# Kernel optimization log

Measured on AMD Instinct MI355X. Metric: run time of the kernel, lower is better.

## Reference

```python
import jax, jax.numpy as jnp
import numpy as np

B, H, N, D = 2, 8, 2048, 64


def setup_inputs() -> dict:
    key = jax.random.key(0)
    kq, kk, kv = jax.random.split(key, 3)
    q = jax.random.normal(kq, (B, H, N, D), dtype=jnp.float32)
    k = jax.random.normal(kk, (B, H, N, D), dtype=jnp.float32)
    v = jax.random.normal(kv, (B, H, N, D), dtype=jnp.float32)
    return {"q": q, "k": k, "v": v}


def _selective_attn(sim):
    # sim: (b, h, i, j). Gate computed from first head, relu'd, SOS unmasked,
    # diagonal zeroed, shifted down one row, cumsum over query rows, subtracted.
    b, h, i, j = sim.shape
    gate = jax.nn.relu(sim[:, 0])                       # (b, i, j)
    gate = gate.at[:, :, j - i].set(0.0)                # no_mask_sos: column -i
    eye = jnp.eye(i, dtype=sim.dtype)
    if j > i:
        eye = jnp.pad(eye, ((0, 0), (j - i, 0)), constant_values=1.0)
    gate = (1.0 - eye) * gate
    # F.pad(gate, (0,0,1,-1)): shift rows down by one, drop last row
    gate = jnp.pad(gate, ((0, 0), (1, 0), (0, 0)))[:, :i, :]
    gate = jnp.cumsum(gate, axis=-2)
    return sim - gate[:, None]                          # broadcast over heads


def reference(q, k, v):
    scale = q.shape[-1] ** -0.5
    i, j = q.shape[-2], k.shape[-2]

    # squared L2 distance scores: ||q||^2 + ||k||^2 - 2 q.k  (== cdist(q,k)**2)
    q_sq = jnp.sum(q * q, axis=-1)                      # (b, h, i)
    k_sq = jnp.sum(k * k, axis=-1)                      # (b, h, j)
    qk = jnp.einsum('bhid,bhjd->bhij', q, k)            # (b, h, i, j)
    d2 = jnp.maximum(q_sq[..., :, None] + k_sq[..., None, :] - 2.0 * qk, 0.0)
    sim = -d2 * scale

    # causal mask (triu with offset j - i + 1)
    mask_value = -jnp.finfo(sim.dtype).max
    causal = jnp.triu(jnp.ones((i, j), dtype=bool), j - i + 1)
    sim = jnp.where(causal, mask_value, sim)

    # selective attention gating
    sim = _selective_attn(sim)

    # one-hot straight-through attention
    idx = jnp.argmax(sim, axis=-1)                      # (b, h, i)
    hard = jax.nn.one_hot(idx, j, dtype=sim.dtype)      # (b, h, i, j)
    soft = jax.nn.softmax(sim, axis=-1)
    attn = hard + soft - jax.lax.stop_gradient(soft)

    return jnp.einsum('bhij,bhjd->bhid', attn, v)
```

## Files before the change

### kernel.cpp

```cpp
#include <hip/hip_runtime.h>
#include <stdint.h>

#define B_ 2
#define H_ 8
#define N_ 2048
#define D_ 64
#define BH_ (B_ * H_)
#define NROWS (BH_ * N_)
#define TPB_ 544
#define TASKS (TPB_ * BH_)
#define EPSF 8e-3f
#define INFF __int_as_float(0x7f800000)

using u64 = unsigned long long;
using u32 = unsigned int;
typedef __attribute__((ext_vector_type(8))) short short8;
typedef __attribute__((ext_vector_type(4))) float f32x4;

#define MFMA16(A, B, C) __builtin_amdgcn_mfma_f32_16x16x32_bf16((A), (B), (C), 0, 0, 0)

__global__ __launch_bounds__(256) void prep_k(
    const float* __restrict__ k, char* __restrict__ khi_g,
    char* __restrict__ klo_g, float* __restrict__ ksq_g,
    u32* __restrict__ count)
{
  if (blockIdx.x == 0 && threadIdx.x == 0) count[0] = 0;
  const int t = (int)blockIdx.x * 256 + threadIdx.x;
  const int r = t >> 3, kg = t & 7;
  const float* kp = k + (size_t)r * D_ + kg * 8;
  const float4 f0 = *(const float4*)kp;
  const float4 f1 = *(const float4*)(kp + 4);
  const float vv[8] = {f0.x, f0.y, f0.z, f0.w, f1.x, f1.y, f1.z, f1.w};
  u32 hw[4], lw[4];
  float ps = 0.f;
  #pragma unroll
  for (int e = 0; e < 4; ++e) {
    const float va = vv[2 * e], vb = vv[2 * e + 1];
    ps = fmaf(va, va, ps); ps = fmaf(vb, vb, ps);
    const u32 ha = __float_as_uint(va) & 0xFFFF0000u;
    const u32 hb = __float_as_uint(vb) & 0xFFFF0000u;
    hw[e] = (ha >> 16) | hb;
    const u32 la = __float_as_uint(va - __uint_as_float(ha));
    const u32 lb = __float_as_uint(vb - __uint_as_float(hb));
    lw[e] = (la >> 16) | (lb & 0xFFFF0000u);
  }
  const size_t off = ((size_t)(r >> 4) * 2 + (kg >> 2)) * 1024 +
                     (size_t)(((kg & 3) << 4) + (r & 15)) * 16;
  *(uint4*)(khi_g + off) = make_uint4(hw[0], hw[1], hw[2], hw[3]);
  *(uint4*)(klo_g + off) = make_uint4(lw[0], lw[1], lw[2], lw[3]);
  float ssum = ps;
  ssum += __shfl_xor(ssum, 1);
  ssum += __shfl_xor(ssum, 2);
  ssum += __shfl_xor(ssum, 4);
  if (kg == 0) ksq_g[r] = ssum;
}

__device__ __forceinline__ void cvt_hilo(const float* p, short8& hi, short8& lo) {
  const float4 f0 = *(const float4*)p;
  const float4 f1 = *(const float4*)(p + 4);
  const float vv[8] = {f0.x, f0.y, f0.z, f0.w, f1.x, f1.y, f1.z, f1.w};
  #pragma unroll
  for (int e = 0; e < 8; ++e) {
    const float v = vv[e];
    const u32 hb = __float_as_uint(v) & 0xFFFF0000u;
    hi[e] = (short)(hb >> 16);
    lo[e] = (short)(__float_as_uint(v - __uint_as_float(hb)) >> 16);
  }
}

__global__ __launch_bounds__(64, 4) void phase1(
    const float* __restrict__ q, const char* __restrict__ khi_g,
    const char* __restrict__ klo_g, const float* __restrict__ ksq_g,
    u64* __restrict__ bestc, u32* __restrict__ secc)
{
  const int b = (int)blockIdx.x;
  const int task = (b & 7) * (TASKS / 8) + (b >> 3);
  const int bh = task / TPB_;
  const int rem = task - bh * TPB_;
  int a = 0;
  while (2 * (a + 1) * (a + 2) <= rem) ++a;
  const int idx = rem - 2 * a * (a + 1);
  const int g2 = 4 * a + idx / (a + 1);
  const int c = idx - (idx / (a + 1)) * (a + 1);
  const int jfirst = c * 8;
  const int jlast = min(jfirst + 7, 2 * g2 + 1);

  const int lane = threadIdx.x & 63;
  const int grp = lane >> 4, c0 = lane & 15;
  const int i0 = g2 * 32;

  short8 ah00, ah01, al00, al01, ah10, ah11, al10, al11;
  {
    const float* q0 = q + ((size_t)bh * N_ + i0 + c0) * D_ + grp * 8;
    cvt_hilo(q0, ah00, al00);
    cvt_hilo(q0 + 32, ah01, al01);
    const float* q1 = q0 + 16 * D_;
    cvt_hilo(q1, ah10, al10);
    cvt_hilo(q1 + 32, ah11, al11);
  }

  float bf[2][4], sf[2][4];
  u32 bj[2][4];
  #pragma unroll
  for (int s = 0; s < 2; ++s)
    #pragma unroll
    for (int r2 = 0; r2 < 4; ++r2) {
      bf[s][r2] = INFF; sf[s][r2] = INFF; bj[s][r2] = 0;
    }

  const size_t fb = (size_t)bh * 128 * 2048;
  const char* ph = khi_g + fb + (size_t)jfirst * 2048 + lane * 16;
  const char* pl = klo_g + fb + (size_t)jfirst * 2048 + lane * 16;
  const float* pk = ksq_g + (size_t)bh * N_ + jfirst * 16 + c0;

  short8 ch0 = *(const short8*)(ph);
  short8 ch1 = *(const short8*)(ph + 1024);
  short8 cl0 = *(const short8*)(pl);
  short8 cl1 = *(const short8*)(pl + 1024);
  float cks = *pk;

  for (int js = jfirst; js <= jlast; ++js) {
    const int adv = (js < jlast) ? 1 : 0;
    const short8 nh0 = *(const short8*)(ph + adv * 2048);
    const short8 nh1 = *(const short8*)(ph + adv * 2048 + 1024);
    const short8 nl0 = *(const short8*)(pl + adv * 2048);
    const short8 nl1 = *(const short8*)(pl + adv * 2048 + 1024);
    const float nks = pk[adv * 16];
    ph += adv * 2048; pl += adv * 2048; pk += adv * 16;

    const int jcol = js * 16 + c0;
    if (js <= 2 * g2) {
      const bool dsub = (js == 2 * g2);
      f32x4 aA = {0.f, 0.f, 0.f, 0.f}, aB = {0.f, 0.f, 0.f, 0.f};
      aA = MFMA16(ah00, ch0, aA);  aB = MFMA16(ah01, ch1, aB);
      aA = MFMA16(ah00, cl0, aA);  aB = MFMA16(ah01, cl1, aB);
      aA = MFMA16(al00, ch0, aA);  aB = MFMA16(al01, ch1, aB);
      #pragma unroll
      for (int reg = 0; reg < 4; ++reg) {
        float score = fmaf(-2.f, aA[reg] + aB[reg], cks);
        if (dsub && jcol > i0 + grp * 4 + reg) score = INFF;
        const float loser = fmaxf(bf[0][reg], score);
        sf[0][reg] = fminf(sf[0][reg], loser);
        if (score < bf[0][reg]) bj[0][reg] = (u32)jcol;
        bf[0][reg] = fminf(bf[0][reg], score);
      }
    }
    {
      const bool dsub = (js == 2 * g2 + 1);
      f32x4 aA = {0.f, 0.f, 0.f, 0.f}, aB = {0.f, 0.f, 0.f, 0.f};
      aA = MFMA16(ah10, ch0, aA);  aB = MFMA16(ah11, ch1, aB);
      aA = MFMA16(ah10, cl0, aA);  aB = MFMA16(ah11, cl1, aB);
      aA = MFMA16(al10, ch0, aA);  aB = MFMA16(al11, ch1, aB);
      #pragma unroll
      for (int reg = 0; reg < 4; ++reg) {
        float score = fmaf(-2.f, aA[reg] + aB[reg], cks);
        if (dsub && jcol > i0 + 16 + grp * 4 + reg) score = INFF;
        const float loser = fmaxf(bf[1][reg], score);
        sf[1][reg] = fminf(sf[1][reg], loser);
        if (score < bf[1][reg]) bj[1][reg] = (u32)jcol;
        bf[1][reg] = fminf(bf[1][reg], score);
      }
    }
    ch0 = nh0; ch1 = nh1; cl0 = nl0; cl1 = nl1; cks = nks;
  }

  #pragma unroll
  for (int s = 0; s < 2; ++s) {
    #pragma unroll
    for (int reg = 0; reg < 4; ++reg) {
      const u32 bbits = __float_as_uint(bf[s][reg]);
      const u32 key = bbits ^ (u32)(((int)bbits >> 31) | 0x80000000);
      u64 pkk = ((u64)key << 32) | bj[s][reg];
      float sv = sf[s][reg];
      #pragma unroll
      for (int m = 1; m < 16; m <<= 1) {
        const u64 opk = (u64)__shfl_xor((long long)pkk, m);
        const float osv = __shfl_xor(sv, m);
        const u32 mk = (u32)(pkk >> 32), ok = (u32)(opk >> 32);
        const u32 lk = (opk < pkk) ? mk : ok;
        const u32 lb = (lk & 0x80000000u) ? (lk ^ 0x80000000u) : ~lk;
        sv = fminf(fminf(sv, osv), __uint_as_float(lb));
        if (opk < pkk) pkk = opk;
      }
      if (c0 == 0) {
        const size_t rr = (size_t)bh * N_ + i0 + s * 16 + grp * 4 + reg;
        bestc[(size_t)c * NROWS + rr] = pkk;
        secc[(size_t)c * NROWS + rr] = __float_as_uint(sv);
      }
    }
  }
}

__global__ __launch_bounds__(256) void combine_gather(
    const u64* __restrict__ bestc, const u32* __restrict__ secc,
    const float* __restrict__ v, float* __restrict__ out,
    u32* __restrict__ flaglist, u32* __restrict__ count)
{
  __shared__ u64 pk_s[4][64];
  __shared__ float s1_s[4][64];
  __shared__ u32 idx_s[64];
  const int tid = threadIdx.x;
  const int r0 = (int)blockIdx.x * 64;
  const int p = tid >> 6, t6 = tid & 63;

  {
    const int r = r0 + t6;
    const int i = r & (N_ - 1);
    const int nch = (2 * (i >> 5) + 9) >> 3;
    u64 b0 = ~0ull;
    float bcur = INFF, s1 = INFF;
    int cstar = -1;
    for (int c2 = p; c2 < nch; c2 += 4) {
      const u64 kk = bestc[(size_t)c2 * NROWS + r];
      const u32 key = (u32)(kk >> 32);
      const u32 bits = (key & 0x80000000u) ? (key ^ 0x80000000u) : ~key;
      const float f = __uint_as_float(bits);
      if (kk < b0) { s1 = fminf(s1, bcur); b0 = kk; bcur = f; cstar = c2; }
      else s1 = fminf(s1, f);
    }
    if (cstar >= 0)
      s1 = fminf(s1, __uint_as_float(secc[(size_t)cstar * NROWS + r]));
    pk_s[p][t6] = b0;
    s1_s[p][t6] = s1;
  }
  __syncthreads();

  if (tid < 64) {
    u64 b0 = ~0ull;
    float bcur = INFF, s1 = INFF;
    #pragma unroll
    for (int pp = 0; pp < 4; ++pp) {
      const u64 kk = pk_s[pp][tid];
      const u32 key = (u32)(kk >> 32);
      const u32 bits = (key & 0x80000000u) ? (key ^ 0x80000000u) : ~key;
      const float f = __uint_as_float(bits);
      if (kk < b0) { s1 = fminf(s1, bcur); b0 = kk; bcur = f; }
      else s1 = fminf(s1, f);
      s1 = fminf(s1, s1_s[pp][tid]);
    }
    idx_s[tid] = (u32)(b0 & 0xFFFFu);
    if ((s1 - bcur) < EPSF) {
      const u32 pos = atomicAdd(count, 1u);
      flaglist[pos] = (u32)(r0 + tid);
    }
  }
  __syncthreads();

  #pragma unroll
  for (int iter = 0; iter < 4; ++iter) {
    const int tk = tid + iter * 256;
    const int rl = tk >> 4, cc = tk & 15;
    const int r = r0 + rl;
    const u32 j = idx_s[rl];
    const int bh = r >> 11;
    const float4 val = ((const float4*)(v + ((size_t)bh * N_ + j) * D_))[cc];
    ((float4*)(out + (size_t)r * D_))[cc] = val;
  }
}

__global__ __launch_bounds__(64) void exact_partial(
    const float* __restrict__ q, const float* __restrict__ k,
    const u32* __restrict__ flaglist, const u32* __restrict__ count,
    double* __restrict__ pd, int* __restrict__ pj)
{
  const int lane = threadIdx.x & 63;
  const int cnt = (int)count[0];
  for (int t = blockIdx.x; (t >> 4) < cnt; t += (int)gridDim.x) {
    const int li = t >> 4, slice = t & 15;
    const int r = (int)flaglist[li];
    const int bh = r >> 11;
    const int i = r & (N_ - 1);
    const int jbase = slice * 128;

    double bbest = 1e300;
    int bjj = 0x7FFFFFFF;
    if (jbase <= i) {
      const float4* qr = (const float4*)(q + (size_t)r * D_);
      float4 qv[16];
      #pragma unroll
      for (int t2 = 0; t2 < 16; ++t2) qv[t2] = qr[t2];
      double s0 = 0, s1 = 0, s2 = 0, s3 = 0;
      #pragma unroll
      for (int t2 = 0; t2 < 16; ++t2) {
        s0 = fma((double)qv[t2].x, (double)qv[t2].x, s0);
        s1 = fma((double)qv[t2].y, (double)qv[t2].y, s1);
        s2 = fma((double)qv[t2].z, (double)qv[t2].z, s2);
        s3 = fma((double)qv[t2].w, (double)qv[t2].w, s3);
      }
      const double qsqd = (s0 + s1) + (s2 + s3);
      const float* kb = k + (size_t)bh * N_ * D_;

      #pragma unroll
      for (int u = 0; u < 2; ++u) {
        const int j = jbase + u * 64 + lane;
        if (j <= i) {
          const float4* kr = (const float4*)(kb + (size_t)j * D_);
          double a0 = 0, a1 = 0, a2 = 0, a3 = 0;
          double t0 = 0, t1 = 0, t2d = 0, t3 = 0;
          #pragma unroll
          for (int t2 = 0; t2 < 16; ++t2) {
            const float4 kv = kr[t2];
            const double k0 = kv.x, k1 = kv.y, k2 = kv.z, k3 = kv.w;
            a0 = fma((double)qv[t2].x, k0, a0);
            a1 = fma((double)qv[t2].y, k1, a1);
            a2 = fma((double)qv[t2].z, k2, a2);
            a3 = fma((double)qv[t2].w, k3, a3);
            t0 = fma(k0, k0, t0);
            t1 = fma(k1, k1, t1);
            t2d = fma(k2, k2, t2d);
            t3 = fma(k3, k3, t3);
          }
          const double raw = (qsqd + ((t0 + t1) + (t2d + t3))) -
                             2.0 * ((a0 + a1) + (a2 + a3));
          const double d2 = raw > 0.0 ? raw : 0.0;
          if (d2 < bbest) { bbest = d2; bjj = j; }
        }
      }
      #pragma unroll
      for (int m = 1; m < 64; m <<= 1) {
        const double ob = __shfl_xor(bbest, m);
        const int oj = __shfl_xor(bjj, m);
        if (ob < bbest || (ob == bbest && oj < bjj)) { bbest = ob; bjj = oj; }
      }
    }
    if (lane == 0) {
      pd[(size_t)li * 16 + slice] = bbest;
      pj[(size_t)li * 16 + slice] = bjj;
    }
  }
}

__global__ __launch_bounds__(64) void exact_final(
    const double* __restrict__ pd, const int* __restrict__ pj,
    const u32* __restrict__ flaglist, const u32* __restrict__ count,
    const float* __restrict__ v, float* __restrict__ out)
{
  const int lane = threadIdx.x & 63;
  const int cnt = (int)count[0];
  for (int li = blockIdx.x; li < cnt; li += (int)gridDim.x) {
    const int r = (int)flaglist[li];
    const int bh = r >> 11;
    double d = (lane < 16) ? pd[(size_t)li * 16 + lane] : 1e300;
    int j = (lane < 16) ? pj[(size_t)li * 16 + lane] : 0x7FFFFFFF;
    #pragma unroll
    for (int m = 1; m < 16; m <<= 1) {
      const double od = __shfl_xor(d, m);
      const int oj = __shfl_xor(j, m);
      if (od < d || (od == d && oj < j)) { d = od; j = oj; }
    }
    if (lane < 16) {
      const float4 val =
          ((const float4*)(v + ((size_t)bh * N_ + j) * D_))[lane];
      ((float4*)(out + (size_t)r * D_))[lane] = val;
    }
  }
}

extern "C" void kernel_launch(void* const* d_in, const int* in_sizes, int n_in,
                              void* d_out, int out_size, void* d_ws,
                              size_t ws_size, hipStream_t stream) {
  const float* q = (const float*)d_in[0];
  const float* k = (const float*)d_in[1];
  const float* v = (const float*)d_in[2];
  float* out = (float*)d_out;

  char* ws = (char*)d_ws;
  u32* count = (u32*)ws;
  u32* flaglist = (u32*)(ws + 4096);
  float* ksq_g = (float*)(ws + 256 * 1024);
  char* khi_g = ws + 1ull * 1024 * 1024;
  char* klo_g = ws + 8ull * 1024 * 1024;
  u64* bestc = (u64*)(ws + 16ull * 1024 * 1024);
  u32* secc = (u32*)(ws + 24ull * 1024 * 1024);
  double* pd = (double*)(ws + 32ull * 1024 * 1024);
  int* pj = (int*)(ws + 40ull * 1024 * 1024);

  prep_k<<<(NROWS * 8) / 256, 256, 0, stream>>>(k, khi_g, klo_g, ksq_g, count);
  phase1<<<TASKS, 64, 0, stream>>>(q, khi_g, klo_g, ksq_g, bestc, secc);
  combine_gather<<<NROWS / 64, 256, 0, stream>>>(bestc, secc, v, out,
                                                 flaglist, count);
  exact_partial<<<2048, 64, 0, stream>>>(q, k, flaglist, count, pd, pj);
  exact_final<<<256, 64, 0, stream>>>(pd, pj, flaglist, count, v, out);
}
```

Measured before the change: 56.79 us.

## Widen phase1 query tile from 32 to 64 rows per wave

Each phase1 wavefront now handles 64 query rows (four 16-row MFMA subtiles) instead of 32, so every K chunk loaded from global memory is reused across twice as many rows. This halves the task count per head and changes the triangular task decomposition and the chunk count used by combine_gather. The cost is more registers for the Q fragments and running best/second state, so the occupancy hint drops from 4 to 3 waves, and there are fewer blocks to keep the GPU busy.

```diff
diff --git a/kernel.cpp b/kernel.cpp
--- a/kernel.cpp
+++ b/kernel.cpp
@@ -7,7 +7,7 @@
 #define D_ 64
 #define BH_ (B_ * H_)
 #define NROWS (BH_ * N_)
-#define TPB_ 544
+#define TPB_ 272
 #define TASKS (TPB_ * BH_)
 #define EPSF 8e-3f
 #define INFF __int_as_float(0x7f800000)
@@ -68,7 +68,7 @@
   }
 }
 
-__global__ __launch_bounds__(64, 4) void phase1(
+__global__ __launch_bounds__(64, 3) void phase1(
     const float* __restrict__ q, const char* __restrict__ khi_g,
     const char* __restrict__ klo_g, const float* __restrict__ ksq_g,
     u64* __restrict__ bestc, u32* __restrict__ secc)
@@ -77,32 +77,32 @@
   const int task = (b & 7) * (TASKS / 8) + (b >> 3);
   const int bh = task / TPB_;
   const int rem = task - bh * TPB_;
-  int a = 0;
-  while (2 * (a + 1) * (a + 2) <= rem) ++a;
-  const int idx = rem - 2 * a * (a + 1);
-  const int g2 = 4 * a + idx / (a + 1);
-  const int c = idx - (idx / (a + 1)) * (a + 1);
+  int t = 0;
+  while ((t + 1) * (t + 2) <= rem) ++t;
+  const int idx = rem - t * (t + 1);
+  const int qn = idx / (t + 1);
+  const int g4 = 2 * t + qn;
+  const int c = idx - qn * (t + 1);
   const int jfirst = c * 8;
-  const int jlast = min(jfirst + 7, 2 * g2 + 1);
+  const int jlast = min(jfirst + 7, 4 * g4 + 3);
 
   const int lane = threadIdx.x & 63;
   const int grp = lane >> 4, c0 = lane & 15;
-  const int i0 = g2 * 32;
-
-  short8 ah00, ah01, al00, al01, ah10, ah11, al10, al11;
-  {
-    const float* q0 = q + ((size_t)bh * N_ + i0 + c0) * D_ + grp * 8;
-    cvt_hilo(q0, ah00, al00);
-    cvt_hilo(q0 + 32, ah01, al01);
-    const float* q1 = q0 + 16 * D_;
-    cvt_hilo(q1, ah10, al10);
-    cvt_hilo(q1 + 32, ah11, al11);
-  }
-
-  float bf[2][4], sf[2][4];
-  u32 bj[2][4];
-  #pragma unroll
-  for (int s = 0; s < 2; ++s)
+  const int i0 = g4 * 64;
+
+  short8 ah[4][2], al[4][2];
+  #pragma unroll
+  for (int s = 0; s < 4; ++s) {
+    const float* qrow =
+        q + ((size_t)bh * N_ + i0 + s * 16 + c0) * D_ + grp * 8;
+    cvt_hilo(qrow, ah[s][0], al[s][0]);
+    cvt_hilo(qrow + 32, ah[s][1], al[s][1]);
+  }
+
+  float bf[4][4], sf[4][4];
+  u32 bj[4][4];
+  #pragma unroll
+  for (int s = 0; s < 4; ++s)
     #pragma unroll
     for (int r2 = 0; r2 < 4; ++r2) {
       bf[s][r2] = INFF; sf[s][r2] = INFF; bj[s][r2] = 0;
@@ -129,43 +129,29 @@
     ph += adv * 2048; pl += adv * 2048; pk += adv * 16;
 
     const int jcol = js * 16 + c0;
-    if (js <= 2 * g2) {
-      const bool dsub = (js == 2 * g2);
+    #pragma unroll
+    for (int s = 0; s < 4; ++s) {
+      if (js > 4 * g4 + s) continue;
+      const bool dsub = (js == 4 * g4 + s);
       f32x4 aA = {0.f, 0.f, 0.f, 0.f}, aB = {0.f, 0.f, 0.f, 0.f};
-      aA = MFMA16(ah00, ch0, aA);  aB = MFMA16(ah01, ch1, aB);
-      aA = MFMA16(ah00, cl0, aA);  aB = MFMA16(ah01, cl1, aB);
-      aA = MFMA16(al00, ch0, aA);  aB = MFMA16(al01, ch1, aB);
+      aA = MFMA16(ah[s][0], ch0, aA);  aB = MFMA16(ah[s][1], ch1, aB);
+      aA = MFMA16(ah[s][0], cl0, aA);  aB = MFMA16(ah[s][1], cl1, aB);
+      aA = MFMA16(al[s][0], ch0, aA);  aB = MFMA16(al[s][1], ch1, aB);
       #pragma unroll
       for (int reg = 0; reg < 4; ++reg) {
         float score = fmaf(-2.f, aA[reg] + aB[reg], cks);
-        if (dsub && jcol > i0 + grp * 4 + reg) score = INFF;
-        const float loser = fmaxf(bf[0][reg], score);
-        sf[0][reg] = fminf(sf[0][reg], loser);
-        if (score < bf[0][reg]) bj[0][reg] = (u32)jcol;
-        bf[0][reg] = fminf(bf[0][reg], score);
-      }
-    }
-    {
-      const bool dsub = (js == 2 * g2 + 1);
-      f32x4 aA = {0.f, 0.f, 0.f, 0.f}, aB = {0.f, 0.f, 0.f, 0.f};
-      aA = MFMA16(ah10, ch0, aA);  aB = MFMA16(ah11, ch1, aB);
-      aA = MFMA16(ah10, cl0, aA);  aB = MFMA16(ah11, cl1, aB);
-      aA = MFMA16(al10, ch0, aA);  aB = MFMA16(al11, ch1, aB);
-      #pragma unroll
-      for (int reg = 0; reg < 4; ++reg) {
-        float score = fmaf(-2.f, aA[reg] + aB[reg], cks);
-        if (dsub && jcol > i0 + 16 + grp * 4 + reg) score = INFF;
-        const float loser = fmaxf(bf[1][reg], score);
-        sf[1][reg] = fminf(sf[1][reg], loser);
-        if (score < bf[1][reg]) bj[1][reg] = (u32)jcol;
-        bf[1][reg] = fminf(bf[1][reg], score);
+        if (dsub && jcol > i0 + s * 16 + grp * 4 + reg) score = INFF;
+        const float loser = fmaxf(bf[s][reg], score);
+        sf[s][reg] = fminf(sf[s][reg], loser);
+        if (score < bf[s][reg]) bj[s][reg] = (u32)jcol;
+        bf[s][reg] = fminf(bf[s][reg], score);
       }
     }
     ch0 = nh0; ch1 = nh1; cl0 = nl0; cl1 = nl1; cks = nks;
   }
 
   #pragma unroll
-  for (int s = 0; s < 2; ++s) {
+  for (int s = 0; s < 4; ++s) {
     #pragma unroll
     for (int reg = 0; reg < 4; ++reg) {
       const u32 bbits = __float_as_uint(bf[s][reg]);
@@ -206,7 +192,7 @@
   {
     const int r = r0 + t6;
     const int i = r & (N_ - 1);
-    const int nch = (2 * (i >> 5) + 9) >> 3;
+    const int nch = ((i >> 6) + 2) >> 1;
     u64 b0 = ~0ull;
     float bcur = INFF, s1 = INFF;
     int cstar = -1;
```

After: 62.82 us. +10.6%, slower.

## Precompute Q bf16 hi/lo fragments and double key chunk size per task

Applied to the files above, without the earlier changes.

The prep kernel now also converts Q into MFMA-ready bf16 hi/lo fragments in workspace, so phase1 loads them directly instead of converting per task. Each phase1 task now covers 16 key tiles instead of 8, which roughly halves the task count (TPB 544 to 288) and the number of partial results combine_gather has to merge. The launch-bounds occupancy hint drops from 4 to 3 waves to leave room for more registers. Longer tasks may worsen load balance across the triangular causal work and add an extra Q write/read pass.

```diff
diff --git a/kernel.cpp b/kernel.cpp
--- a/kernel.cpp
+++ b/kernel.cpp
@@ -7,7 +7,7 @@
 #define D_ 64
 #define BH_ (B_ * H_)
 #define NROWS (BH_ * N_)
-#define TPB_ 544
+#define TPB_ 288
 #define TASKS (TPB_ * BH_)
 #define EPSF 8e-3f
 #define INFF __int_as_float(0x7f800000)
@@ -19,85 +19,103 @@
 
 #define MFMA16(A, B, C) __builtin_amdgcn_mfma_f32_16x16x32_bf16((A), (B), (C), 0, 0, 0)
 
-__global__ __launch_bounds__(256) void prep_k(
-    const float* __restrict__ k, char* __restrict__ khi_g,
-    char* __restrict__ klo_g, float* __restrict__ ksq_g,
+__global__ __launch_bounds__(256) void prep_all(
+    const float* __restrict__ q, const float* __restrict__ k,
+    char* __restrict__ khi_g, char* __restrict__ klo_g,
+    float* __restrict__ ksq_g, char* __restrict__ qfrag,
     u32* __restrict__ count)
 {
-  if (blockIdx.x == 0 && threadIdx.x == 0) count[0] = 0;
-  const int t = (int)blockIdx.x * 256 + threadIdx.x;
-  const int r = t >> 3, kg = t & 7;
-  const float* kp = k + (size_t)r * D_ + kg * 8;
-  const float4 f0 = *(const float4*)kp;
-  const float4 f1 = *(const float4*)(kp + 4);
-  const float vv[8] = {f0.x, f0.y, f0.z, f0.w, f1.x, f1.y, f1.z, f1.w};
-  u32 hw[4], lw[4];
-  float ps = 0.f;
-  #pragma unroll
-  for (int e = 0; e < 4; ++e) {
-    const float va = vv[2 * e], vb = vv[2 * e + 1];
-    ps = fmaf(va, va, ps); ps = fmaf(vb, vb, ps);
-    const u32 ha = __float_as_uint(va) & 0xFFFF0000u;
-    const u32 hb = __float_as_uint(vb) & 0xFFFF0000u;
-    hw[e] = (ha >> 16) | hb;
-    const u32 la = __float_as_uint(va - __uint_as_float(ha));
-    const u32 lb = __float_as_uint(vb - __uint_as_float(hb));
-    lw[e] = (la >> 16) | (lb & 0xFFFF0000u);
-  }
-  const size_t off = ((size_t)(r >> 4) * 2 + (kg >> 2)) * 1024 +
-                     (size_t)(((kg & 3) << 4) + (r & 15)) * 16;
-  *(uint4*)(khi_g + off) = make_uint4(hw[0], hw[1], hw[2], hw[3]);
-  *(uint4*)(klo_g + off) = make_uint4(lw[0], lw[1], lw[2], lw[3]);
-  float ssum = ps;
-  ssum += __shfl_xor(ssum, 1);
-  ssum += __shfl_xor(ssum, 2);
-  ssum += __shfl_xor(ssum, 4);
-  if (kg == 0) ksq_g[r] = ssum;
-}
-
-__device__ __forceinline__ void cvt_hilo(const float* p, short8& hi, short8& lo) {
-  const float4 f0 = *(const float4*)p;
-  const float4 f1 = *(const float4*)(p + 4);
-  const float vv[8] = {f0.x, f0.y, f0.z, f0.w, f1.x, f1.y, f1.z, f1.w};
-  #pragma unroll
-  for (int e = 0; e < 8; ++e) {
-    const float v = vv[e];
-    const u32 hb = __float_as_uint(v) & 0xFFFF0000u;
-    hi[e] = (short)(hb >> 16);
-    lo[e] = (short)(__float_as_uint(v - __uint_as_float(hb)) >> 16);
-  }
-}
-
-__global__ __launch_bounds__(64, 4) void phase1(
-    const float* __restrict__ q, const char* __restrict__ khi_g,
+  const int blk = (int)blockIdx.x;
+  if (blk < 1024) {
+    if (blk == 0 && threadIdx.x == 0) count[0] = 0;
+    const int t = blk * 256 + threadIdx.x;
+    const int r = t >> 3, kg = t & 7;
+    const float* kp = k + (size_t)r * D_ + kg * 8;
+    const float4 f0 = *(const float4*)kp;
+    const float4 f1 = *(const float4*)(kp + 4);
+    const float vv[8] = {f0.x, f0.y, f0.z, f0.w, f1.x, f1.y, f1.z, f1.w};
+    u32 hw[4], lw[4];
+    float ps = 0.f;
+    #pragma unroll
+    for (int e = 0; e < 4; ++e) {
+      const float va = vv[2 * e], vb = vv[2 * e + 1];
+      ps = fmaf(va, va, ps); ps = fmaf(vb, vb, ps);
+      const u32 ha = __float_as_uint(va) & 0xFFFF0000u;
+      const u32 hb = __float_as_uint(vb) & 0xFFFF0000u;
+      hw[e] = (ha >> 16) | hb;
+      const u32 la = __float_as_uint(va - __uint_as_float(ha));
+      const u32 lb = __float_as_uint(vb - __uint_as_float(hb));
+      lw[e] = (la >> 16) | (lb & 0xFFFF0000u);
+    }
+    const size_t off = ((size_t)(r >> 4) * 2 + (kg >> 2)) * 1024 +
+                       (size_t)(((kg & 3) << 4) + (r & 15)) * 16;
+    *(uint4*)(khi_g + off) = make_uint4(hw[0], hw[1], hw[2], hw[3]);
+    *(uint4*)(klo_g + off) = make_uint4(lw[0], lw[1], lw[2], lw[3]);
+    float ssum = ps;
+    ssum += __shfl_xor(ssum, 1);
+    ssum += __shfl_xor(ssum, 2);
+    ssum += __shfl_xor(ssum, 4);
+    if (kg == 0) ksq_g[r] = ssum;
+  } else {
+    const int t2 = (blk - 1024) * 256 + threadIdx.x;
+    const int l = t2 & 63;
+    const int p = (t2 >> 6) & 3;
+    const int grp = (t2 >> 8) & 127;
+    const int bh = t2 >> 15;
+    const int h = p & 1, islo = p >> 1;
+    const int row = bh * N_ + grp * 16 + (l & 15);
+    const float* src = q + (size_t)row * D_ + h * 32 + (l >> 4) * 8;
+    const float4 f0 = *(const float4*)src;
+    const float4 f1 = *(const float4*)(src + 4);
+    const float vv[8] = {f0.x, f0.y, f0.z, f0.w, f1.x, f1.y, f1.z, f1.w};
+    u32 wds[4];
+    #pragma unroll
+    for (int e = 0; e < 4; ++e) {
+      const float va = vv[2 * e], vb = vv[2 * e + 1];
+      const u32 ha = __float_as_uint(va) & 0xFFFF0000u;
+      const u32 hb = __float_as_uint(vb) & 0xFFFF0000u;
+      if (islo) {
+        const u32 la = __float_as_uint(va - __uint_as_float(ha));
+        const u32 lb = __float_as_uint(vb - __uint_as_float(hb));
+        wds[e] = (la >> 16) | (lb & 0xFFFF0000u);
+      } else {
+        wds[e] = (ha >> 16) | hb;
+      }
+    }
+    const size_t off = ((((size_t)bh * 128 + grp) * 4 + p) * 64 + l) * 16;
+    *(uint4*)(qfrag + off) = make_uint4(wds[0], wds[1], wds[2], wds[3]);
+  }
+}
+
+__global__ __launch_bounds__(64, 3) void phase1(
+    const char* __restrict__ qfrag, const char* __restrict__ khi_g,
     const char* __restrict__ klo_g, const float* __restrict__ ksq_g,
     u64* __restrict__ bestc, u32* __restrict__ secc)
 {
   const int b = (int)blockIdx.x;
   const int task = (b & 7) * (TASKS / 8) + (b >> 3);
   const int bh = task / TPB_;
-  const int rem = task - bh * TPB_;
-  int a = 0;
-  while (2 * (a + 1) * (a + 2) <= rem) ++a;
-  const int idx = rem - 2 * a * (a + 1);
-  const int g2 = 4 * a + idx / (a + 1);
-  const int c = idx - (idx / (a + 1)) * (a + 1);
-  const int jfirst = c * 8;
-  const int jlast = min(jfirst + 7, 2 * g2 + 1);
+  int rem = task - bh * TPB_;
+  int g2 = 0, nc = 1;
+  while (rem >= nc) { rem -= nc; ++g2; nc = (2 * g2 + 17) >> 4; }
+  const int c = rem;
+  const int jfirst = c * 16;
+  const int jlast = min(jfirst + 15, 2 * g2 + 1);
 
   const int lane = threadIdx.x & 63;
   const int grp = lane >> 4, c0 = lane & 15;
   const int i0 = g2 * 32;
 
-  short8 ah00, ah01, al00, al01, ah10, ah11, al10, al11;
-  {
-    const float* q0 = q + ((size_t)bh * N_ + i0 + c0) * D_ + grp * 8;
-    cvt_hilo(q0, ah00, al00);
-    cvt_hilo(q0 + 32, ah01, al01);
-    const float* q1 = q0 + 16 * D_;
-    cvt_hilo(q1, ah10, al10);
-    cvt_hilo(q1 + 32, ah11, al11);
-  }
+  const char* qb =
+      qfrag + ((((size_t)bh * 128 + g2 * 2) * 4) * 64 + lane) * 16;
+  const short8 ah00 = *(const short8*)(qb);
+  const short8 ah01 = *(const short8*)(qb + 1024);
+  const short8 al00 = *(const short8*)(qb + 2048);
+  const short8 al01 = *(const short8*)(qb + 3072);
+  const short8 ah10 = *(const short8*)(qb + 4096);
+  const short8 ah11 = *(const short8*)(qb + 4096 + 1024);
+  const short8 al10 = *(const short8*)(qb + 4096 + 2048);
+  const short8 al11 = *(const short8*)(qb + 4096 + 3072);
 
   float bf[2][4], sf[2][4];
   u32 bj[2][4];
@@ -206,7 +224,7 @@
   {
     const int r = r0 + t6;
     const int i = r & (N_ - 1);
-    const int nch = (2 * (i >> 5) + 9) >> 3;
+    const int nch = (2 * (i >> 5) + 17) >> 4;
     u64 b0 = ~0ull;
     float bcur = INFF, s1 = INFF;
     int cstar = -1;
@@ -374,9 +392,10 @@
   u32* secc = (u32*)(ws + 24ull * 1024 * 1024);
   double* pd = (double*)(ws + 32ull * 1024 * 1024);
   int* pj = (int*)(ws + 40ull * 1024 * 1024);
-
-  prep_k<<<(NROWS * 8) / 256, 256, 0, stream>>>(k, khi_g, klo_g, ksq_g, count);
-  phase1<<<TASKS, 64, 0, stream>>>(q, khi_g, klo_g, ksq_g, bestc, secc);
+  char* qfrag = ws + 44ull * 1024 * 1024;
+
+  prep_all<<<3072, 256, 0, stream>>>(q, k, khi_g, klo_g, ksq_g, qfrag, count);
+  phase1<<<TASKS, 64, 0, stream>>>(qfrag, khi_g, klo_g, ksq_g, bestc, secc);
   combine_gather<<<NROWS / 64, 256, 0, stream>>>(bestc, secc, v, out,
                                                  flaglist, count);
   exact_partial<<<2048, 64, 0, stream>>>(q, k, flaglist, count, pd, pj);
```

New measurement: 56.09 us. Within noise of the previous version (-1.2%).

## Use 16-tile column chunks in phase1 and fuse exact fallback kernels

Applied to the files above, without the earlier changes.

Phase1 tasks now cover up to 16 key tiles instead of 8, which roughly halves the task count and the per-chunk candidate writes that combine_gather must merge. The task decode becomes a simple loop, and occupancy is lowered to 3 waves. The explicit register double-buffering of the next K tile is removed in favour of direct loads. The exact_partial and exact_final kernels are merged into one 1024-thread block that reduces the 16 slices through shared memory, dropping one launch and the partial-result round trip. The trade-off is less parallelism per row group in phase1 and possible load latency exposure without prefetch.

```diff
diff --git a/kernel.cpp b/kernel.cpp
--- a/kernel.cpp
+++ b/kernel.cpp
@@ -7,7 +7,7 @@
 #define D_ 64
 #define BH_ (B_ * H_)
 #define NROWS (BH_ * N_)
-#define TPB_ 544
+#define TPB_ 288
 #define TASKS (TPB_ * BH_)
 #define EPSF 8e-3f
 #define INFF __int_as_float(0x7f800000)
@@ -68,7 +68,7 @@
   }
 }
 
-__global__ __launch_bounds__(64, 4) void phase1(
+__global__ __launch_bounds__(64, 3) void phase1(
     const float* __restrict__ q, const char* __restrict__ khi_g,
     const char* __restrict__ klo_g, const float* __restrict__ ksq_g,
     u64* __restrict__ bestc, u32* __restrict__ secc)
@@ -76,14 +76,12 @@
   const int b = (int)blockIdx.x;
   const int task = (b & 7) * (TASKS / 8) + (b >> 3);
   const int bh = task / TPB_;
-  const int rem = task - bh * TPB_;
-  int a = 0;
-  while (2 * (a + 1) * (a + 2) <= rem) ++a;
-  const int idx = rem - 2 * a * (a + 1);
-  const int g2 = 4 * a + idx / (a + 1);
-  const int c = idx - (idx / (a + 1)) * (a + 1);
-  const int jfirst = c * 8;
-  const int jlast = min(jfirst + 7, 2 * g2 + 1);
+  int rem = task - bh * TPB_;
+  int g2 = 0, nc = 1;
+  while (rem >= nc) { rem -= nc; ++g2; nc = (2 * g2 + 17) >> 4; }
+  const int c = rem;
+  const int jfirst = c * 16;
+  const int jlast = min(jfirst + 15, 2 * g2 + 1);
 
   const int lane = threadIdx.x & 63;
   const int grp = lane >> 4, c0 = lane & 15;
@@ -113,20 +111,13 @@
   const char* pl = klo_g + fb + (size_t)jfirst * 2048 + lane * 16;
   const float* pk = ksq_g + (size_t)bh * N_ + jfirst * 16 + c0;
 
-  short8 ch0 = *(const short8*)(ph);
-  short8 ch1 = *(const short8*)(ph + 1024);
-  short8 cl0 = *(const short8*)(pl);
-  short8 cl1 = *(const short8*)(pl + 1024);
-  float cks = *pk;
-
   for (int js = jfirst; js <= jlast; ++js) {
-    const int adv = (js < jlast) ? 1 : 0;
-    const short8 nh0 = *(const short8*)(ph + adv * 2048);
-    const short8 nh1 = *(const short8*)(ph + adv * 2048 + 1024);
-    const short8 nl0 = *(const short8*)(pl + adv * 2048);
-    const short8 nl1 = *(const short8*)(pl + adv * 2048 + 1024);
-    const float nks = pk[adv * 16];
-    ph += adv * 2048; pl += adv * 2048; pk += adv * 16;
+    const short8 ch0 = *(const short8*)(ph);
+    const short8 ch1 = *(const short8*)(ph + 1024);
+    const short8 cl0 = *(const short8*)(pl);
+    const short8 cl1 = *(const short8*)(pl + 1024);
+    const float cks = *pk;
+    ph += 2048; pl += 2048; pk += 16;
 
     const int jcol = js * 16 + c0;
     if (js <= 2 * g2) {
@@ -161,7 +152,6 @@
         bf[1][reg] = fminf(bf[1][reg], score);
       }
     }
-    ch0 = nh0; ch1 = nh1; cl0 = nl0; cl1 = nl1; cks = nks;
   }
 
   #pragma unroll
@@ -206,7 +196,7 @@
   {
     const int r = r0 + t6;
     const int i = r & (N_ - 1);
-    const int nch = (2 * (i >> 5) + 9) >> 3;
+    const int nch = (2 * (i >> 5) + 17) >> 4;
     u64 b0 = ~0ull;
     float bcur = INFF, s1 = INFF;
     int cstar = -1;
@@ -258,19 +248,22 @@
   }
 }
 
-__global__ __launch_bounds__(64) void exact_partial(
+__global__ __launch_bounds__(1024) void exact_fused(
     const float* __restrict__ q, const float* __restrict__ k,
-    const u32* __restrict__ flaglist, const u32* __restrict__ count,
-    double* __restrict__ pd, int* __restrict__ pj)
+    const float* __restrict__ v, float* __restrict__ out,
+    const u32* __restrict__ flaglist, const u32* __restrict__ count)
 {
-  const int lane = threadIdx.x & 63;
+  __shared__ double sd[16];
+  __shared__ int sj[16];
+  const int tid = threadIdx.x;
+  const int w = tid >> 6;
+  const int lane = tid & 63;
   const int cnt = (int)count[0];
-  for (int t = blockIdx.x; (t >> 4) < cnt; t += (int)gridDim.x) {
-    const int li = t >> 4, slice = t & 15;
+  for (int li = blockIdx.x; li < cnt; li += (int)gridDim.x) {
     const int r = (int)flaglist[li];
     const int bh = r >> 11;
     const int i = r & (N_ - 1);
-    const int jbase = slice * 128;
+    const int jbase = w * 128;
 
     double bbest = 1e300;
     int bjj = 0x7FFFFFFF;
@@ -323,36 +316,25 @@
         if (ob < bbest || (ob == bbest && oj < bjj)) { bbest = ob; bjj = oj; }
       }
     }
-    if (lane == 0) {
-      pd[(size_t)li * 16 + slice] = bbest;
-      pj[(size_t)li * 16 + slice] = bjj;
-    }
-  }
-}
-
-__global__ __launch_bounds__(64) void exact_final(
-    const double* __restrict__ pd, const int* __restrict__ pj,
-    const u32* __restrict__ flaglist, const u32* __restrict__ count,
-    const float* __restrict__ v, float* __restrict__ out)
-{
-  const int lane = threadIdx.x & 63;
-  const int cnt = (int)count[0];
-  for (int li = blockIdx.x; li < cnt; li += (int)gridDim.x) {
-    const int r = (int)flaglist[li];
-    const int bh = r >> 11;
-    double d = (lane < 16) ? pd[(size_t)li * 16 + lane] : 1e300;
-    int j = (lane < 16) ? pj[(size_t)li * 16 + lane] : 0x7FFFFFFF;
-    #pragma unroll
-    for (int m = 1; m < 16; m <<= 1) {
-      const double od = __shfl_xor(d, m);
-      const int oj = __shfl_xor(j, m);
-      if (od < d || (od == d && oj < j)) { d = od; j = oj; }
-    }
-    if (lane < 16) {
-      const float4 val =
-          ((const float4*)(v + ((size_t)bh * N_ + j) * D_))[lane];
-      ((float4*)(out + (size_t)r * D_))[lane] = val;
-    }
+    if (lane == 0) { sd[w] = bbest; sj[w] = bjj; }
+    __syncthreads();
+
+    if (w == 0) {
+      double d = (lane < 16) ? sd[lane] : 1e300;
+      int j = (lane < 16) ? sj[lane] : 0x7FFFFFFF;
+      #pragma unroll
+      for (int m = 1; m < 16; m <<= 1) {
+        const double od = __shfl_xor(d, m);
+        const int oj = __shfl_xor(j, m);
+        if (od < d || (od == d && oj < j)) { d = od; j = oj; }
+      }
+      if (lane < 16) {
+        const float4 val =
+            ((const float4*)(v + ((size_t)bh * N_ + j) * D_))[lane];
+        ((float4*)(out + (size_t)r * D_))[lane] = val;
+      }
+    }
+    __syncthreads();
   }
 }
 
@@ -372,13 +354,10 @@
   char* klo_g = ws + 8ull * 1024 * 1024;
   u64* bestc = (u64*)(ws + 16ull * 1024 * 1024);
   u32* secc = (u32*)(ws + 24ull * 1024 * 1024);
-  double* pd = (double*)(ws + 32ull * 1024 * 1024);
-  int* pj = (int*)(ws + 40ull * 1024 * 1024);
 
   prep_k<<<(NROWS * 8) / 256, 256, 0, stream>>>(k, khi_g, klo_g, ksq_g, count);
   phase1<<<TASKS, 64, 0, stream>>>(q, khi_g, klo_g, ksq_g, bestc, secc);
   combine_gather<<<NROWS / 64, 256, 0, stream>>>(bestc, secc, v, out,
                                                  flaglist, count);
-  exact_partial<<<2048, 64, 0, stream>>>(q, k, flaglist, count, pd, pj);
-  exact_final<<<256, 64, 0, stream>>>(pd, pj, flaglist, count, v, out);
-}
+  exact_fused<<<256, 1024, 0, stream>>>(q, k, v, out, flaglist, count);
+}
```

New measurement: 80.09 us. +41.0%, slower.
